# Performance work log

Hardware: AMD Instinct MI355X
Metric: run time of the kernel (lower is better)

Reference implementation:

```python
import jax, jax.numpy as jnp
import numpy as np


def setup_inputs() -> dict:
    key = jax.random.key(0)
    ks = jax.random.split(key, 32)
    def rn(i, shape, s=0.02):
        return jax.random.normal(ks[i], shape, dtype=jnp.float32) * s
    z = lambda n: jnp.zeros((n,), dtype=jnp.float32)
    return {
        'c2': rn(0, (8, 256, 112, 112), 1.0),
        'c3': rn(1, (8, 512, 56, 56), 1.0),
        'c4': rn(2, (8, 1024, 28, 28), 1.0),
        'c5': rn(3, (8, 2048, 14, 14), 1.0),
        'lat_w0': rn(4, (256, 256)),  'lat_b0': z(256),
        'lat_w1': rn(5, (512, 256)),  'lat_b1': z(256),
        'lat_w2': rn(6, (1024, 256)), 'lat_b2': z(256),
        'lat_w3': rn(7, (2048, 256)), 'lat_b3': z(256),
        'sp_w1': rn(8, (2048, 512)), 'sp_b1': z(512),
        'sp_w2': rn(9, (512, 4)),    'sp_b2': z(4),
        'qkv_w': rn(10, (256, 768)), 'qkv_b': z(768),
        'proj_w': rn(11, (256, 256)), 'proj_b': z(256),
        'gat_W': rn(12, (4, 256, 256)),
        'gat_a': rn(13, (4, 512)),
        'out_w': rn(14, (1024, 256)), 'out_b': z(256),
        'label_emb': rn(15, (80, 256), 1.0),
        'spec_w1': rn(16, (256, 128)), 'spec_b1': z(128),
        'spec_w2': rn(17, (128, 80)),  'spec_b2': z(80),
        'spat_w1': rn(18, (256, 128)), 'spat_b1': z(128),
        'spat_w2': rn(19, (128, 80)),  'spat_b2': z(80),
        'gate_w': rn(20, (256, 80)), 'gate_b': z(80),
        'unc_w': rn(21, (256, 80)),  'unc_b': z(80),
    }


def _forward(c2, c3, c4, c5,
             lat_w0, lat_b0, lat_w1, lat_b1, lat_w2, lat_b2, lat_w3, lat_b3,
             sp_w1, sp_b1, sp_w2, sp_b2,
             qkv_w, qkv_b, proj_w, proj_b,
             gat_W, gat_a, out_w, out_b, label_emb,
             spec_w1, spec_b1, spec_w2, spec_b2,
             spat_w1, spat_b1, spat_w2, spat_b2,
             gate_w, gate_b, unc_w, unc_b):
    B = c2.shape[0]
    L = label_emb.shape[0]
    C = 256
    # --- DynamicScaleAwareFPN ---
    pooled = c5.mean(axis=(2, 3))                                   # [B,2048]
    sw = jax.nn.softmax(jax.nn.relu(pooled @ sp_w1 + sp_b1) @ sp_w2 + sp_b2, axis=1)  # [B,4]
    H, W = c2.shape[2], c2.shape[3]
    feats = (c2, c3, c4, c5)
    lws = (lat_w0, lat_w1, lat_w2, lat_w3)
    lbs = (lat_b0, lat_b1, lat_b2, lat_b3)
    fused = jnp.zeros((B, C, H, W), dtype=c2.dtype)
    for i in range(4):  # fixed 4 scales
        l = jnp.einsum('bchw,cd->bdhw', feats[i], lws[i]) + lbs[i][None, :, None, None]
        if l.shape[2] != H or l.shape[3] != W:
            l = jax.image.resize(l, (B, C, H, W), method='bilinear')  # align_corners=False
        fused = fused + l * sw[:, i, None, None, None]
    # --- DeformableAttention (N=H*W > max_tokens=196 -> adaptive pool to 14x14) ---
    th = 14
    x = fused.reshape(B, C, th, H // th, th, W // th).mean(axis=(3, 5))  # exact adaptive avg pool
    x = x.reshape(B, C, th * th).transpose(0, 2, 1)                      # [B,196,C]
    N, nh, hd = th * th, 8, C // 8
    qkv = (x @ qkv_w + qkv_b).reshape(B, N, 3, nh, hd).transpose(2, 0, 3, 1, 4)
    q, k, v = qkv[0], qkv[1], qkv[2]                                     # [B,nh,N,hd]
    attn = jax.nn.softmax(jnp.einsum('bhnd,bhmd->bhnm', q, k) * (hd ** -0.5), axis=-1)
    xo = jnp.einsum('bhnm,bhmd->bhnd', attn, v).transpose(0, 2, 1, 3).reshape(B, N, C)
    xo = xo @ proj_w + proj_b
    gctx = xo.mean(axis=1)                                               # [B,C]
    # --- CrossLabelSemanticGraph (4 GAT heads) ---
    lf = label_emb[None] + gctx[:, None, :]                              # [B,L,C]
    def gat(Wm, avec):
        Wx = lf @ Wm                                                     # [B,L,C]
        # a([Wx_i ; Wx_j]) = Wx_i @ a1 + Wx_j @ a2  (avoids O(L^2*2C) tensor)
        s1 = Wx @ avec[:C]                                               # [B,L]
        s2 = Wx @ avec[C:]                                               # [B,L]
        e = jax.nn.leaky_relu(s1[:, :, None] + s2[:, None, :], 0.2)      # [B,L,L]
        att = jax.nn.softmax(e, axis=2)
        return att @ Wx, att
    heads, atts = jax.vmap(gat)(gat_W, gat_a)                            # [4,B,L,C],[4,B,L,L]
    concat = jnp.moveaxis(heads, 0, 2).reshape(B, L, 4 * C)              # head-order concat
    graph = concat @ out_w + out_b                                       # [B,L,C]
    agg = graph.mean(axis=1)                                             # [B,C]
    # --- SpectralSpatialFusion (dropout inactive at eval) ---
    spec = jax.nn.relu(agg @ spec_w1 + spec_b1) @ spec_w2 + spec_b2
    spat = jax.nn.relu(agg @ spat_w1 + spat_b1) @ spat_w2 + spat_b2
    gate = jax.nn.sigmoid(agg @ gate_w + gate_b)
    logits = gate * spec + (1.0 - gate) * spat
    # --- UncertaintyHead ---
    alpha = jax.nn.softplus(agg @ unc_w + unc_b) + 1.0
    unc = L / jnp.sum(alpha, axis=1, keepdims=True)
    return (logits, spec, spat, gate, unc, sw, atts)


def reference(c2, c3, c4, c5,
              lat_w0, lat_b0, lat_w1, lat_b1, lat_w2, lat_b2, lat_w3, lat_b3,
              sp_w1, sp_b1, sp_w2, sp_b2,
              qkv_w, qkv_b, proj_w, proj_b,
              gat_W, gat_a, out_w, out_b, label_emb,
              spec_w1, spec_b1, spec_w2, spec_b2,
              spat_w1, spat_b1, spat_w2, spat_b2,
              gate_w, gate_b, unc_w, unc_b):
    return _forward(c2, c3, c4, c5,
                    lat_w0, lat_b0, lat_w1, lat_b1, lat_w2, lat_b2, lat_w3, lat_b3,
                    sp_w1, sp_b1, sp_w2, sp_b2,
                    qkv_w, qkv_b, proj_w, proj_b,
                    gat_W, gat_a, out_w, out_b, label_emb,
                    spec_w1, spec_b1, spec_w2, spec_b2,
                    spat_w1, spat_b1, spat_w2, spat_b2,
                    gate_w, gate_b, unc_w, unc_b)
```

## Files before the change

kernel.cpp:

```cpp
#include <hip/hip_runtime.h>
#include <math.h>

typedef __attribute__((ext_vector_type(8))) short bshort8;
typedef __attribute__((ext_vector_type(4))) float f32x4;

#define DI __device__ __forceinline__

DI unsigned short f2bf(float x) {
    unsigned int u = __builtin_bit_cast(unsigned int, x);
    u += 0x7fffu + ((u >> 16) & 1u);
    return (unsigned short)(u >> 16);
}

DI bshort8 pack8(const float* v) {
    bshort8 r;
    #pragma unroll
    for (int j = 0; j < 8; j++) r[j] = (short)f2bf(v[j]);
    return r;
}

DI f32x4 mfma16(bshort8 a, bshort8 b, f32x4 c) {
    return __builtin_amdgcn_mfma_f32_16x16x32_bf16(a, b, c, 0, 0, 0);
}

__device__ const float W14[14][3] = {
    {0.875f, 0.125f, 0.f},
    {0.125f, 0.75f, 0.125f}, {0.125f, 0.75f, 0.125f}, {0.125f, 0.75f, 0.125f},
    {0.125f, 0.75f, 0.125f}, {0.125f, 0.75f, 0.125f}, {0.125f, 0.75f, 0.125f},
    {0.125f, 0.75f, 0.125f}, {0.125f, 0.75f, 0.125f}, {0.125f, 0.75f, 0.125f},
    {0.125f, 0.75f, 0.125f}, {0.125f, 0.75f, 0.125f}, {0.125f, 0.75f, 0.125f},
    {0.125f, 0.875f, 0.f}};
__device__ const float W28[14][4] = {
    {0.5f, 0.4375f, 0.0625f, 0.f},
    {0.0625f, 0.4375f, 0.4375f, 0.0625f}, {0.0625f, 0.4375f, 0.4375f, 0.0625f},
    {0.0625f, 0.4375f, 0.4375f, 0.0625f}, {0.0625f, 0.4375f, 0.4375f, 0.0625f},
    {0.0625f, 0.4375f, 0.4375f, 0.0625f}, {0.0625f, 0.4375f, 0.4375f, 0.0625f},
    {0.0625f, 0.4375f, 0.4375f, 0.0625f}, {0.0625f, 0.4375f, 0.4375f, 0.0625f},
    {0.0625f, 0.4375f, 0.4375f, 0.0625f}, {0.0625f, 0.4375f, 0.4375f, 0.0625f},
    {0.0625f, 0.4375f, 0.4375f, 0.0625f}, {0.0625f, 0.4375f, 0.4375f, 0.0625f},
    {0.0625f, 0.4375f, 0.5f, 0.f}};
__device__ const float W56[14][6] = {
    {0.25f, 0.25f, 0.25f, 0.21875f, 0.03125f, 0.f},
    {0.03125f, 0.21875f, 0.25f, 0.25f, 0.21875f, 0.03125f},
    {0.03125f, 0.21875f, 0.25f, 0.25f, 0.21875f, 0.03125f},
    {0.03125f, 0.21875f, 0.25f, 0.25f, 0.21875f, 0.03125f},
    {0.03125f, 0.21875f, 0.25f, 0.25f, 0.21875f, 0.03125f},
    {0.03125f, 0.21875f, 0.25f, 0.25f, 0.21875f, 0.03125f},
    {0.03125f, 0.21875f, 0.25f, 0.25f, 0.21875f, 0.03125f},
    {0.03125f, 0.21875f, 0.25f, 0.25f, 0.21875f, 0.03125f},
    {0.03125f, 0.21875f, 0.25f, 0.25f, 0.21875f, 0.03125f},
    {0.03125f, 0.21875f, 0.25f, 0.25f, 0.21875f, 0.03125f},
    {0.03125f, 0.21875f, 0.25f, 0.25f, 0.21875f, 0.03125f},
    {0.03125f, 0.21875f, 0.25f, 0.25f, 0.21875f, 0.03125f},
    {0.03125f, 0.21875f, 0.25f, 0.25f, 0.21875f, 0.03125f},
    {0.03125f, 0.21875f, 0.25f, 0.25f, 0.25f, 0.f}};

template <int N, int C, int TAPS>
DI void pool_body(const float* __restrict__ src, unsigned short* __restrict__ dst,
                  unsigned blk, unsigned t)
{
    unsigned id = blk * 256u + t;
    unsigned p = id / 196u;
    unsigned r = id - p * 196u;
    unsigned ti = r / 14u, tj = r - ti * 14u;
    unsigned b = p / C, cin = p - b * C;
    const float* plane = src + (size_t)p * (N * N);
    float acc = 0.f;
    if constexpr (N == 112) {
        const float4* p4 = (const float4*)(plane + (size_t)(ti * 8) * 112 + tj * 8);
        float4 rv[16];
        #pragma unroll
        for (int i = 0; i < 8; i++) { rv[2 * i] = p4[i * 28]; rv[2 * i + 1] = p4[i * 28 + 1]; }
        #pragma unroll
        for (int i = 0; i < 16; i++) acc += (rv[i].x + rv[i].y) + (rv[i].z + rv[i].w);
        acc *= (1.f / 64.f);
    } else {
        constexpr int STRIDE = N / 14;
        const float (*WT)[TAPS] = (N == 14) ? (const float (*)[TAPS])W14
                                : (N == 28) ? (const float (*)[TAPS])W28
                                            : (const float (*)[TAPS])W56;
        int hs = (int)(STRIDE * ti) - 1; if (hs < 0) hs = 0;
        int ws = (int)(STRIDE * tj) - 1; if (ws < 0) ws = 0;
        float wh[TAPS], ww[TAPS];
        #pragma unroll
        for (int i = 0; i < TAPS; i++) { wh[i] = WT[ti][i]; ww[i] = WT[tj][i]; }
        float rv[TAPS][TAPS];
        #pragma unroll
        for (int i = 0; i < TAPS; i++) {
            int hi = hs + i; if (hi > N - 1) hi = N - 1;
            const float* row = plane + (size_t)hi * N;
            #pragma unroll
            for (int j = 0; j < TAPS; j++) {
                int wj = ws + j; if (wj > N - 1) wj = N - 1;
                rv[i][j] = row[wj];
            }
        }
        #pragma unroll
        for (int i = 0; i < TAPS; i++) {
            float rs = 0.f;
            #pragma unroll
            for (int j = 0; j < TAPS; j++) rs += ww[j] * rv[i][j];
            acc += wh[i] * rs;
        }
    }
    dst[(size_t)cin * 1568 + b * 196 + r] = f2bf(acc);
}

DI void c5_mean_body(const float* __restrict__ c5, float* __restrict__ pooled,
                     unsigned blk, unsigned t)
{
    int wid = t >> 6, lane = t & 63;
    int p = blk * 4 + wid;
    const float* plane = c5 + (size_t)p * 196;
    float v = plane[lane] + plane[64 + lane] + plane[128 + lane];
    if (lane < 4) v += plane[192 + lane];
    #pragma unroll
    for (int off = 32; off > 0; off >>= 1) v += __shfl_xor(v, off, 64);
    if (lane == 0) pooled[p] = v * (1.f / 196.f);
}

__global__ __launch_bounds__(256) void pool_all(
    const float* __restrict__ c2, const float* __restrict__ c3,
    const float* __restrict__ c4, const float* __restrict__ c5,
    unsigned short* __restrict__ pf0, unsigned short* __restrict__ pf1,
    unsigned short* __restrict__ pf2, unsigned short* __restrict__ pf3,
    float* __restrict__ pooled)
{
    unsigned bx = blockIdx.x, t = threadIdx.x;
    if (bx < 1568u)       pool_body<112, 256, 8>(c2, pf0, bx, t);
    else if (bx < 4704u)  pool_body<56, 512, 6>(c3, pf1, bx - 1568u, t);
    else if (bx < 10976u) pool_body<28, 1024, 4>(c4, pf2, bx - 4704u, t);
    else if (bx < 23520u) pool_body<14, 2048, 3>(c5, pf3, bx - 10976u, t);
    else                  c5_mean_body(c5, pooled, bx - 23520u, t);
}

__global__ __launch_bounds__(512) void sw_part(
    const float* __restrict__ pooled, const float* __restrict__ sp_w1,
    float* __restrict__ partial,
    const float* __restrict__ gat_W, const float* __restrict__ gat_a,
    float* __restrict__ Wa)
{
    int t = threadIdx.x;
    if (blockIdx.y >= 8) {
        int e = (blockIdx.y - 8) * 8 + blockIdx.x;
        int h = e >> 2, q = e & 3;
        __shared__ float a1[256], a2[256];
        if (t < 256) { a1[t] = gat_a[h * 512 + t]; a2[t] = gat_a[h * 512 + 256 + t]; }
        __syncthreads();
        int w = t >> 6, lane = t & 63;
        #pragma unroll
        for (int ci = 0; ci < 8; ci++) {
            int c = q * 64 + w * 8 + ci;
            const float* row = gat_W + (size_t)h * 65536 + (size_t)c * 256;
            float p1 = 0.f, p2 = 0.f;
            #pragma unroll
            for (int jj = 0; jj < 4; jj++) {
                float v = row[lane + 64 * jj];
                p1 += v * a1[lane + 64 * jj];
                p2 += v * a2[lane + 64 * jj];
            }
            #pragma unroll
            for (int off = 32; off > 0; off >>= 1) {
                p1 += __shfl_xor(p1, off, 64);
                p2 += __shfl_xor(p2, off, 64);
            }
            if (lane == 0) { Wa[h * 512 + c] = p1; Wa[h * 512 + 256 + c] = p2; }
        }
        return;
    }
    int b = blockIdx.x, kc = blockIdx.y;
    __shared__ float ps[256];
    if (t < 256) ps[t] = pooled[b * 2048 + kc * 256 + t];
    __syncthreads();
    float acc = 0.f;
    const float* w = sp_w1 + (size_t)(kc * 256) * 512 + t;
    #pragma unroll 8
    for (int c = 0; c < 256; c++) acc += ps[c] * w[(size_t)c * 512];
    partial[((size_t)b * 8 + kc) * 512 + t] = acc;
}

__global__ __launch_bounds__(512) void sw_fin(
    const float* __restrict__ partial, const float* __restrict__ sp_b1,
    const float* __restrict__ sp_w2, const float* __restrict__ sp_b2,
    const float* __restrict__ lb0, const float* __restrict__ lb1,
    const float* __restrict__ lb2, const float* __restrict__ lb3,
    const float* __restrict__ lemb, const float* __restrict__ Wa,
    float* __restrict__ sw_out, float* __restrict__ xtok,
    float* __restrict__ ldot)
{
    int b = blockIdx.x, t = threadIdx.x;
    __shared__ float h[512];
    __shared__ float s4s[4];
    __shared__ float swl[4];
    __shared__ float bf_s[256];
    float a = sp_b1[t];
    #pragma unroll
    for (int kc = 0; kc < 8; kc++) a += partial[((size_t)b * 8 + kc) * 512 + t];
    h[t] = fmaxf(a, 0.f);
    __syncthreads();
    int wv = t >> 6, lane = t & 63;
    if (wv < 4) {
        float acc = 0.f;
        #pragma unroll
        for (int i = 0; i < 8; i++) {
            int idx = lane + 64 * i;
            acc += h[idx] * sp_w2[idx * 4 + wv];
        }
        #pragma unroll
        for (int off = 32; off > 0; off >>= 1) acc += __shfl_xor(acc, off, 64);
        if (lane == 0) s4s[wv] = acc + sp_b2[wv];
    }
    __syncthreads();
    if (t == 0) {
        float mx = fmaxf(fmaxf(s4s[0], s4s[1]), fmaxf(s4s[2], s4s[3]));
        float e0 = expf(s4s[0] - mx), e1 = expf(s4s[1] - mx);
        float e2 = expf(s4s[2] - mx), e3 = expf(s4s[3] - mx);
        float inv = 1.f / (e0 + e1 + e2 + e3);
        swl[0] = e0 * inv; swl[1] = e1 * inv; swl[2] = e2 * inv; swl[3] = e3 * inv;
        for (int o = 0; o < 4; o++) sw_out[b * 4 + o] = swl[o];
    }
    __syncthreads();
    if (t < 256)
        bf_s[t] = swl[0] * lb0[t] + swl[1] * lb1[t] + swl[2] * lb2[t] + swl[3] * lb3[t];
    {
        int pair = t >> 6;
        #pragma unroll
        for (int r = 0; r < 10; r++) {
            int l = b * 10 + r;
            const float* le = lemb + l * 256 + lane * 4;
            const float* wa = Wa + pair * 256 + lane * 4;
            float p = le[0] * wa[0] + le[1] * wa[1] + le[2] * wa[2] + le[3] * wa[3];
            #pragma unroll
            for (int off = 32; off > 0; off >>= 1) p += __shfl_xor(p, off, 64);
            if (lane == 0) ldot[l * 8 + pair] = p;
        }
    }
    __syncthreads();
    int c = t & 255, half = t >> 8;
    float bv = bf_s[c];
    float* xb = xtok + (size_t)b * 196 * 256 + c;
    for (int r = half; r < 196; r += 2) xb[(size_t)r * 256] = bv;
}

__global__ __launch_bounds__(256) void lateral_slice(
    const unsigned short* __restrict__ pf0, const unsigned short* __restrict__ pf1,
    const unsigned short* __restrict__ pf2, const unsigned short* __restrict__ pf3,
    const float* __restrict__ w0, const float* __restrict__ w1,
    const float* __restrict__ w2, const float* __restrict__ w3,
    const float* __restrict__ sw, float* __restrict__ xtok)
{
    const int sArr[8]    = {0, 1, 2, 2, 3, 3, 3, 3};
    const int koffArr[8] = {0, 0, 0, 512, 0, 512, 1024, 1536};
    const int klenArr[8] = {256, 512, 512, 512, 512, 512, 512, 512};
    int sl = blockIdx.y;
    int s = sArr[sl], koff = koffArr[sl], klen = klenArr[sl];
    const unsigned short* pf = (s == 0) ? pf0 : (s == 1) ? pf1 : (s == 2) ? pf2 : pf3;
    const float* W  = (s == 0) ? w0  : (s == 1) ? w1  : (s == 2) ? w2  : w3;

    int mt = blockIdx.x % 49, nt = blockIdx.x / 49;
    int m0 = mt * 32, n0 = nt * 64;
    __shared__ alignas(16) unsigned short As[1024];
    __shared__ alignas(16) unsigned short Bs[2048];
    int t = threadIdx.x, lane = t & 63, wid = t >> 6;
    int wm = wid >> 1, wn = wid & 1;
    f32x4 acc0 = {0, 0, 0, 0}, acc1 = {0, 0, 0, 0};

    int f = t & 63;
    int mA = m0 + ((t >> 6) & 1) * 16 + (f & 15);
    int kbA = (f >> 4) * 8;
    int nB = n0 + (t >> 6) * 16 + (f & 15);
    int kbB = (f >> 4) * 8;

    unsigned short ark[8];
    float br[8];
    auto loadA = [&](int k0) {
        if (t < 128) {
            const unsigned short* base = pf + (size_t)(koff + k0 + kbA) * 1568 + mA;
            #pragma unroll
            for (int j = 0; j < 8; j++) ark[j] = base[(size_t)j * 1568];
        }
    };
    auto loadB = [&](int k0) {
        const float* base = W + (size_t)(koff + k0 + kbB) * 256 + nB;
        #pragma unroll
        for (int j = 0; j < 8; j++) br[j] = base[(size_t)j * 256];
    };

    loadA(0); loadB(0);
    for (int k0 = 0; k0 < klen; k0 += 32) {
        if (t < 128) {
            bshort8 v8;
            #pragma unroll
            for (int j = 0; j < 8; j++) v8[j] = (short)ark[j];
            *(bshort8*)&As[(((t >> 6) & 1) * 512 + f * 8)] = v8;
        }
        *(bshort8*)&Bs[((t >> 6) * 512 + f * 8)] = pack8(br);
        __syncthreads();
        if (k0 + 32 < klen) { loadA(k0 + 32); loadB(k0 + 32); }
        bshort8 av = *(const bshort8*)&As[wm * 512 + lane * 8];
        bshort8 bv0 = *(const bshort8*)&Bs[(wn * 2 + 0) * 512 + lane * 8];
        bshort8 bv1 = *(const bshort8*)&Bs[(wn * 2 + 1) * 512 + lane * 8];
        acc0 = mfma16(av, bv0, acc0);
        acc1 = mfma16(av, bv1, acc1);
        __syncthreads();
    }
    int col0 = n0 + wn * 32 + (lane & 15);
    int rbase = m0 + wm * 16 + ((lane >> 4) << 2);
    #pragma unroll
    for (int r = 0; r < 4; r++) {
        int m = rbase + r;
        float swv = sw[(m / 196) * 4 + s];
        atomicAdd(&xtok[(size_t)m * 256 + col0], acc0[r] * swv);
        atomicAdd(&xtok[(size_t)m * 256 + col0 + 16], acc1[r] * swv);
    }
}

template <bool B_IS_KXN>
__global__ __launch_bounds__(256) void gemm_kernel(
    const float* __restrict__ Ab, int lda, long long sAy, long long sAz,
    const float* __restrict__ Bb, int ldb, long long sBy, long long sBz,
    float* __restrict__ Cb, int ldc, long long sCy, long long sCz,
    const float* __restrict__ bias, int M, int N, int K,
    float alpha, int mtiles)
{
    const float* A = Ab + blockIdx.y * sAy + blockIdx.z * sAz;
    const float* B = Bb + blockIdx.y * sBy + blockIdx.z * sBz;
    float* C = Cb + blockIdx.y * sCy + blockIdx.z * sCz;
    int mt = blockIdx.x % mtiles, nt = blockIdx.x / mtiles;
    int m0 = mt * 32, n0 = nt * 64;
    __shared__ alignas(16) unsigned short As[1024];
    __shared__ alignas(16) unsigned short Bs[2048];
    int t = threadIdx.x, lane = t & 63, wid = t >> 6;
    int wm = wid >> 1, wn = wid & 1;
    f32x4 acc0 = {0, 0, 0, 0}, acc1 = {0, 0, 0, 0};

    int f = t & 63;
    int mA = m0 + ((t >> 6) & 1) * 16 + (f & 15);
    int kbA = (f >> 4) * 8;
    int nB = n0 + (t >> 6) * 16 + (f & 15);
    int kbB = (f >> 4) * 8;

    float ar[8], br[8];
    auto loadA = [&](int k0) {
        if (t < 128) {
            int kb = k0 + kbA;
            if (mA < M && kb + 8 <= K) {
                const float4* p = (const float4*)(A + (size_t)mA * lda + kb);
                float4 u = p[0], v = p[1];
                ar[0] = u.x; ar[1] = u.y; ar[2] = u.z; ar[3] = u.w;
                ar[4] = v.x; ar[5] = v.y; ar[6] = v.z; ar[7] = v.w;
            } else {
                #pragma unroll
                for (int j = 0; j < 8; j++) {
                    int k = kb + j;
                    ar[j] = (mA < M && k < K) ? A[(size_t)mA * lda + k] : 0.f;
                }
            }
        }
    };
    auto loadB = [&](int k0) {
        int kb = k0 + kbB;
        if constexpr (B_IS_KXN) {
            #pragma unroll
            for (int j = 0; j < 8; j++) {
                int k = kb + j;
                br[j] = (k < K && nB < N) ? B[(size_t)k * ldb + nB] : 0.f;
            }
        } else {
            if (nB < N && kb + 8 <= K) {
                const float4* p = (const float4*)(B + (size_t)nB * ldb + kb);
                float4 u = p[0], v = p[1];
                br[0] = u.x; br[1] = u.y; br[2] = u.z; br[3] = u.w;
                br[4] = v.x; br[5] = v.y; br[6] = v.z; br[7] = v.w;
            } else {
                #pragma unroll
                for (int j = 0; j < 8; j++) {
                    int k = kb + j;
                    br[j] = (nB < N && k < K) ? B[(size_t)nB * ldb + k] : 0.f;
                }
            }
        }
    };

    loadA(0); loadB(0);
    for (int k0 = 0; k0 < K; k0 += 32) {
        if (t < 128) *(bshort8*)&As[(((t >> 6) & 1) * 512 + f * 8)] = pack8(ar);
        *(bshort8*)&Bs[((t >> 6) * 512 + f * 8)] = pack8(br);
        __syncthreads();
        if (k0 + 32 < K) { loadA(k0 + 32); loadB(k0 + 32); }
        bshort8 av = *(const bshort8*)&As[wm * 512 + lane * 8];
        bshort8 bv0 = *(const bshort8*)&Bs[(wn * 2 + 0) * 512 + lane * 8];
        bshort8 bv1 = *(const bshort8*)&Bs[(wn * 2 + 1) * 512 + lane * 8];
        acc0 = mfma16(av, bv0, acc0);
        acc1 = mfma16(av, bv1, acc1);
        __syncthreads();
    }
    int col0 = n0 + wn * 32 + (lane & 15);
    int rbase = m0 + wm * 16 + ((lane >> 4) << 2);
    #pragma unroll
    for (int r = 0; r < 4; r++) {
        int m = rbase + r;
        if (m < M) {
            if (col0 < N) {
                float v = acc0[r] * alpha;
                if (bias) v += bias[col0];
                C[(size_t)m * ldc + col0] = v;
            }
            int c1 = col0 + 16;
            if (c1 < N) {
                float v = acc1[r] * alpha;
                if (bias) v += bias[c1];
                C[(size_t)m * ldc + c1] = v;
            }
        }
    }
}

__global__ __launch_bounds__(256) void fused_attn(
    const float* __restrict__ qkv, float* __restrict__ xo)
{
    int mt = blockIdx.x, h = blockIdx.y, b = blockIdx.z;
    const float* Qb = qkv + (size_t)b * 150528 + h * 32;
    const float* Kb = Qb + 256;
    const float* Vb = Qb + 512;

    __shared__ alignas(16) unsigned short As[1024];
    __shared__ alignas(16) unsigned short Bs[2048];
    __shared__ float Ss[32 * 256];

    int t = threadIdx.x, lane = t & 63, wid = t >> 6;
    int wm = wid >> 1, wn = wid & 1;
    int f = t & 63;
    int m0 = mt * 32;

    if (t < 128) {
        float ar[8];
        int mA = m0 + ((t >> 6) & 1) * 16 + (f & 15);
        int kb = (f >> 4) * 8;
        if (mA < 196) {
            const float4* p = (const float4*)(Qb + (size_t)mA * 768 + kb);
            float4 u = p[0], v = p[1];
            ar[0] = u.x; ar[1] = u.y; ar[2] = u.z; ar[3] = u.w;
            ar[4] = v.x; ar[5] = v.y; ar[6] = v.z; ar[7] = v.w;
        } else {
            #pragma unroll
            for (int j = 0; j < 8; j++) ar[j] = 0.f;
        }
        *(bshort8*)&As[(((t >> 6) & 1) * 512 + f * 8)] = pack8(ar);
    }

    {
        int nBl = (t >> 6) * 16 + (f & 15);
        int kbB = (f >> 4) * 8;
        float br[8];
        auto loadB = [&](int g) {
            int key = g * 64 + nBl;
            if (key < 196) {
                const float4* p = (const float4*)(Kb + (size_t)key * 768 + kbB);
                float4 u = p[0], v = p[1];
                br[0] = u.x; br[1] = u.y; br[2] = u.z; br[3] = u.w;
                br[4] = v.x; br[5] = v.y; br[6] = v.z; br[7] = v.w;
            } else {
                #pragma unroll
                for (int j = 0; j < 8; j++) br[j] = 0.f;
            }
        };
        loadB(0);
        for (int g = 0; g < 4; g++) {
            __syncthreads();
            *(bshort8*)&Bs[((t >> 6) * 512 + f * 8)] = pack8(br);
            __syncthreads();
            if (g < 3) loadB(g + 1);
            f32x4 acc0 = {0, 0, 0, 0}, acc1 = {0, 0, 0, 0};
            bshort8 av = *(const bshort8*)&As[wm * 512 + lane * 8];
            bshort8 bv0 = *(const bshort8*)&Bs[(wn * 2 + 0) * 512 + lane * 8];
            bshort8 bv1 = *(const bshort8*)&Bs[(wn * 2 + 1) * 512 + lane * 8];
            acc0 = mfma16(av, bv0, acc0);
            acc1 = mfma16(av, bv1, acc1);
            int col0 = g * 64 + wn * 32 + (lane & 15);
            int rbase = wm * 16 + ((lane >> 4) << 2);
            #pragma unroll
            for (int r = 0; r < 4; r++) {
                Ss[(rbase + r) * 256 + col0]      = acc0[r] * 0.17677669529663687f;
                Ss[(rbase + r) * 256 + col0 + 16] = acc1[r] * 0.17677669529663687f;
            }
        }
    }
    __syncthreads();

    {
        #pragma unroll
        for (int i = 0; i < 8; i++) {
            float* p = Ss + (wid * 8 + i) * 256;
            float v0 = p[lane], v1 = p[64 + lane], v2 = p[128 + lane];
            float v3 = (lane < 4) ? p[192 + lane] : -1e30f;
            float mx = fmaxf(fmaxf(v0, v1), fmaxf(v2, v3));
            #pragma unroll
            for (int off = 32; off > 0; off >>= 1) mx = fmaxf(mx, __shfl_xor(mx, off, 64));
            float e0 = expf(v0 - mx), e1 = expf(v1 - mx), e2 = expf(v2 - mx);
            float e3 = (lane < 4) ? expf(v3 - mx) : 0.f;
            float sum = e0 + e1 + e2 + e3;
            #pragma unroll
            for (int off = 32; off > 0; off >>= 1) sum += __shfl_xor(sum, off, 64);
            float inv = 1.f / sum;
            p[lane] = e0 * inv;
            p[64 + lane] = e1 * inv;
            p[128 + lane] = e2 * inv;
            if (lane < 4) p[192 + lane] = e3 * inv;
            else          p[192 + lane] = 0.f;
        }
    }
    __syncthreads();

    {
        f32x4 acc0 = {0, 0, 0, 0}, acc1 = {0, 0, 0, 0};
        int nBl = (t >> 6) * 16 + (f & 15);
        int kbB = (f >> 4) * 8;
        int mAl = ((t >> 6) & 1) * 16 + (f & 15);
        int kbA = (f >> 4) * 8;
        float ar[8], br[8];
        auto loadA = [&](int k0) {
            if (t < 128) {
                #pragma unroll
                for (int j = 0; j < 8; j++) ar[j] = Ss[mAl * 256 + k0 + kbA + j];
            }
        };
        auto loadB = [&](int k0) {
            #pragma unroll
            for (int j = 0; j < 8; j++) {
                int k = k0 + kbB + j;
                br[j] = (k < 196 && nBl < 32) ? Vb[(size_t)k * 768 + nBl] : 0.f;
            }
        };
        loadA(0); loadB(0);
        for (int k0 = 0; k0 < 256; k0 += 32) {
            __syncthreads();
            if (t < 128) *(bshort8*)&As[(((t >> 6) & 1) * 512 + f * 8)] = pack8(ar);
            *(bshort8*)&Bs[((t >> 6) * 512 + f * 8)] = pack8(br);
            __syncthreads();
            if (k0 + 32 < 256) { loadA(k0 + 32); loadB(k0 + 32); }
            bshort8 av = *(const bshort8*)&As[wm * 512 + lane * 8];
            bshort8 bv0 = *(const bshort8*)&Bs[(wn * 2 + 0) * 512 + lane * 8];
            bshort8 bv1 = *(const bshort8*)&Bs[(wn * 2 + 1) * 512 + lane * 8];
            acc0 = mfma16(av, bv0, acc0);
            acc1 = mfma16(av, bv1, acc1);
        }
        int col0 = wn * 32 + (lane & 15);
        int rbase = wm * 16 + ((lane >> 4) << 2);
        if (col0 < 32) {
            #pragma unroll
            for (int r = 0; r < 4; r++) {
                int m = m0 + rbase + r;
                if (m < 196) {
                    xo[((size_t)b * 196 + m) * 256 + h * 32 + col0]      = acc0[r];
                    xo[((size_t)b * 196 + m) * 256 + h * 32 + col0 + 16] = acc1[r];
                }
            }
        }
    }
}

__global__ __launch_bounds__(1024) void tail1(
    const float* __restrict__ xo, const float* __restrict__ proj_w,
    const float* __restrict__ proj_b,
    const float* __restrict__ gat_W, const float* __restrict__ lemb,
    const float* __restrict__ Wa, const float* __restrict__ ldot,
    float* __restrict__ atts, float* __restrict__ hm_g)
{
    int b = blockIdx.x >> 2, h = blockIdx.x & 3;
    int t = threadIdx.x, lane = t & 63, wv = t >> 6;
    __shared__ float red[1024];
    __shared__ float xm[256];
    __shared__ float gctx_s[256];
    __shared__ float gdot_s[2];
    __shared__ float s12h[160];
    __shared__ float am_s[80];
    __shared__ float av_s[256];

    {
        int c = t & 255, sl = t >> 8;
        const float* base = xo + ((size_t)b * 196 + sl * 49) * 256 + c;
        float s = 0.f;
        #pragma unroll 7
        for (int i = 0; i < 49; i++) s += base[(size_t)i * 256];
        red[t] = s;
    }
    if (t < 80) am_s[t] = 0.f;
    __syncthreads();
    if (t < 256) xm[t] = (red[t] + red[256 + t] + red[512 + t] + red[768 + t]) * (1.f / 196.f);
    __syncthreads();

    {
        int n = t & 255, ks = t >> 8;
        float acc = 0.f;
        const float* w = proj_w + (size_t)(ks * 64) * 256 + n;
        #pragma unroll 8
        for (int i = 0; i < 64; i++) acc += xm[ks * 64 + i] * w[(size_t)i * 256];
        red[t] = acc;
    }
    __syncthreads();
    if (t < 256) gctx_s[t] = proj_b[t] + red[t] + red[256 + t] + red[512 + t] + red[768 + t];
    __syncthreads();

    if (wv < 2) {
        int pair = h * 2 + wv;
        const float* wa = Wa + pair * 256 + lane * 4;
        float p = gctx_s[lane * 4] * wa[0] + gctx_s[lane * 4 + 1] * wa[1]
                + gctx_s[lane * 4 + 2] * wa[2] + gctx_s[lane * 4 + 3] * wa[3];
        #pragma unroll
        for (int off = 32; off > 0; off >>= 1) p += __shfl_xor(p, off, 64);
        if (lane == 0) gdot_s[wv] = p;
    }
    __syncthreads();
    if (t < 160) {
        int q = t / 80, l = t - q * 80;
        s12h[t] = ldot[l * 8 + h * 2 + q] + gdot_s[q];
    }
    __syncthreads();

    {
        #pragma unroll
        for (int rr = 0; rr < 5; rr++) {
            int i = rr * 16 + wv;
            float s1i = s12h[i];
            const float* s2 = s12h + 80;
            float v0 = s1i + s2[lane]; v0 = v0 > 0.f ? v0 : 0.2f * v0;
            float v1 = -1e30f;
            if (lane < 16) { v1 = s1i + s2[64 + lane]; v1 = v1 > 0.f ? v1 : 0.2f * v1; }
            float mx = fmaxf(v0, v1);
            #pragma unroll
            for (int off = 32; off > 0; off >>= 1) mx = fmaxf(mx, __shfl_xor(mx, off, 64));
            float e0 = expf(v0 - mx), e1 = (lane < 16) ? expf(v1 - mx) : 0.f;
            float sum = e0 + e1;
            #pragma unroll
            for (int off = 32; off > 0; off >>= 1) sum += __shfl_xor(sum, off, 64);
            float inv = 1.f / sum;
            float* orow = atts + (size_t)h * 51200 + b * 6400 + i * 80;
            float p0 = e0 * inv;
            orow[lane] = p0;
            atomicAdd(&am_s[lane], p0);
            if (lane < 16) {
                float p1 = e1 * inv;
                orow[64 + lane] = p1;
                atomicAdd(&am_s[64 + lane], p1);
            }
        }
    }
    __syncthreads();

    {
        int n = t & 255, ks = t >> 8;
        float acc = 0.f;
        const float* le = lemb + n;
        #pragma unroll 5
        for (int l = ks * 20; l < ks * 20 + 20; l++) acc += am_s[l] * le[(size_t)l * 256];
        red[t] = acc;
    }
    __syncthreads();
    if (t < 256)
        av_s[t] = (red[t] + red[256 + t] + red[512 + t] + red[768 + t]) * (1.f / 80.f)
                + gctx_s[t];
    __syncthreads();
    {
        int n = t & 255, ks = t >> 8;
        float acc = 0.f;
        const float* w = gat_W + (size_t)h * 65536 + (size_t)(ks * 64) * 256 + n;
        #pragma unroll 8
        for (int i = 0; i < 64; i++) acc += av_s[ks * 64 + i] * w[(size_t)i * 256];
        red[t] = acc;
    }
    __syncthreads();
    if (t < 256)
        hm_g[(b * 4 + h) * 256 + t] = red[t] + red[256 + t] + red[512 + t] + red[768 + t];
}

__global__ __launch_bounds__(1024) void tail2(
    const float* __restrict__ hm_g,
    const float* __restrict__ out_w, const float* __restrict__ out_b,
    const float* __restrict__ spec_w1, const float* __restrict__ spec_b1,
    const float* __restrict__ spec_w2, const float* __restrict__ spec_b2,
    const float* __restrict__ spat_w1, const float* __restrict__ spat_b1,
    const float* __restrict__ spat_w2, const float* __restrict__ spat_b2,
    const float* __restrict__ gate_w, const float* __restrict__ gate_b,
    const float* __restrict__ unc_w, const float* __restrict__ unc_b,
    float* __restrict__ out)
{
    int b = blockIdx.x, t = threadIdx.x;
    __shared__ float red[1024];
    __shared__ float as_s[256];
    __shared__ float hb_s[256];
    __shared__ float fv_s[320];

    {
        int n = t & 255, ks = t >> 8;
        float acc = 0.f;
        const float* hv = hm_g + b * 1024 + ks * 256;
        const float* w = out_w + (size_t)(ks * 256) * 256 + n;
        #pragma unroll 8
        for (int k = 0; k < 256; k++) acc += hv[k] * w[(size_t)k * 256];
        red[t] = acc;
    }
    __syncthreads();
    if (t < 256) as_s[t] = out_b[t] + red[t] + red[256 + t] + red[512 + t] + red[768 + t];
    __syncthreads();

    {
        int u = t & 255, ks = t >> 8;
        int which = u >> 7, oo = u & 127;
        const float* w1 = which ? spat_w1 : spec_w1;
        float acc = 0.f;
        #pragma unroll 8
        for (int i = 0; i < 64; i++) {
            int k = ks * 64 + i;
            acc += as_s[k] * w1[(size_t)k * 128 + oo];
        }
        red[t] = acc;
    }
    __syncthreads();
    if (t < 256) {
        int which = t >> 7, oo = t & 127;
        const float* b1 = which ? spat_b1 : spec_b1;
        hb_s[t] = fmaxf(red[t] + red[256 + t] + red[512 + t] + red[768 + t] + b1[oo], 0.f);
    }
    __syncthreads();

    if (t < 960) {
        int sub = t / 320, u = t - sub * 320;
        int head = u / 80, o = u - head * 80;
        const float* wp; const float* src; int K;
        if (head == 0)      { wp = spec_w2; src = hb_s;       K = 128; }
        else if (head == 1) { wp = spat_w2; src = hb_s + 128; K = 128; }
        else if (head == 2) { wp = gate_w;  src = as_s;       K = 256; }
        else                { wp = unc_w;   src = as_s;       K = 256; }
        int k0 = (K * sub) / 3, k1 = (K * (sub + 1)) / 3;
        float acc = 0.f;
        for (int k = k0; k < k1; k++) acc += src[k] * wp[(size_t)k * 80 + o];
        red[sub * 320 + u] = acc;
    }
    __syncthreads();
    if (t < 320) {
        int head = t / 80, o = t - head * 80;
        const float* bp = head == 0 ? spec_b2 : head == 1 ? spat_b2 : head == 2 ? gate_b : unc_b;
        fv_s[t] = red[t] + red[320 + t] + red[640 + t] + bp[o];
    }
    __syncthreads();

    if (t < 80) {
        float sp = fv_s[t], st2 = fv_s[80 + t], gz = fv_s[160 + t], uz = fv_s[240 + t];
        float g = 1.f / (1.f + expf(-gz));
        out[b * 80 + t] = g * sp + (1.f - g) * st2;
        out[640 + b * 80 + t] = sp;
        out[1280 + b * 80 + t] = st2;
        out[1920 + b * 80 + t] = g;
        red[t] = log1pf(expf(uz)) + 1.f;
    }
    __syncthreads();
    if (t == 0) {
        float s = 0.f;
        for (int l = 0; l < 80; l++) s += red[l];
        out[2560 + b] = 80.f / s;
    }
}

extern "C" void kernel_launch(void* const* d_in, const int* in_sizes, int n_in,
                              void* d_out, int out_size, void* d_ws, size_t ws_size,
                              hipStream_t stream)
{
    (void)in_sizes; (void)n_in; (void)out_size; (void)ws_size;
    const float* c2 = (const float*)d_in[0];
    const float* c3 = (const float*)d_in[1];
    const float* c4 = (const float*)d_in[2];
    const float* c5 = (const float*)d_in[3];
    const float* lat_w0 = (const float*)d_in[4];
    const float* lat_b0 = (const float*)d_in[5];
    const float* lat_w1 = (const float*)d_in[6];
    const float* lat_b1 = (const float*)d_in[7];
    const float* lat_w2 = (const float*)d_in[8];
    const float* lat_b2 = (const float*)d_in[9];
    const float* lat_w3 = (const float*)d_in[10];
    const float* lat_b3 = (const float*)d_in[11];
    const float* sp_w1 = (const float*)d_in[12];
    const float* sp_b1 = (const float*)d_in[13];
    const float* sp_w2 = (const float*)d_in[14];
    const float* sp_b2 = (const float*)d_in[15];
    const float* qkv_w = (const float*)d_in[16];
    const float* qkv_b = (const float*)d_in[17];
    const float* proj_w = (const float*)d_in[18];
    const float* proj_b = (const float*)d_in[19];
    const float* gat_W = (const float*)d_in[20];
    const float* gat_a = (const float*)d_in[21];
    const float* out_w = (const float*)d_in[22];
    const float* out_b = (const float*)d_in[23];
    const float* label_emb = (const float*)d_in[24];
    const float* spec_w1 = (const float*)d_in[25];
    const float* spec_b1 = (const float*)d_in[26];
    const float* spec_w2 = (const float*)d_in[27];
    const float* spec_b2 = (const float*)d_in[28];
    const float* spat_w1 = (const float*)d_in[29];
    const float* spat_b1 = (const float*)d_in[30];
    const float* spat_w2 = (const float*)d_in[31];
    const float* spat_b2 = (const float*)d_in[32];
    const float* gate_w = (const float*)d_in[33];
    const float* gate_b = (const float*)d_in[34];
    const float* unc_w = (const float*)d_in[35];
    const float* unc_b = (const float*)d_in[36];

    float* out = (float*)d_out;
    float* ws = (float*)d_ws;

    unsigned short* pf0 = (unsigned short*)(ws + 0);
    unsigned short* pf1 = (unsigned short*)(ws + 401408);
    unsigned short* pf2 = (unsigned short*)(ws + 1204224);
    unsigned short* pf3 = (unsigned short*)(ws + 2809856);
    float* pooled = ws + 6021120;
    float* swpart = ws + 6039552;
    float* Wa     = ws + 6072320;
    float* ldot   = ws + 6074368;
    float* qkv    = ws + 0;
    float* xo     = ws + 3662848;
    float* hm_g   = ws + 4253696;
    float* xtok   = ws + 6106112;

    float* swp  = out + 2568;
    float* atts = out + 2600;

    pool_all<<<27616, 256, 0, stream>>>(c2, c3, c4, c5, pf0, pf1, pf2, pf3, pooled);
    sw_part<<<dim3(8, 10), 512, 0, stream>>>(pooled, sp_w1, swpart, gat_W, gat_a, Wa);
    sw_fin<<<8, 512, 0, stream>>>(swpart, sp_b1, sp_w2, sp_b2,
                                  lat_b0, lat_b1, lat_b2, lat_b3,
                                  label_emb, Wa, swp, xtok, ldot);
    lateral_slice<<<dim3(196, 8), 256, 0, stream>>>(pf0, pf1, pf2, pf3,
                                                    lat_w0, lat_w1, lat_w2, lat_w3,
                                                    swp, xtok);
    gemm_kernel<true><<<dim3(49 * 12, 1, 1), 256, 0, stream>>>(
        xtok, 256, 0, 0, qkv_w, 768, 0, 0, qkv, 768, 0, 0,
        qkv_b, 1568, 768, 256, 1.f, 49);
    fused_attn<<<dim3(7, 8, 8), 256, 0, stream>>>(qkv, xo);
    tail1<<<32, 1024, 0, stream>>>(xo, proj_w, proj_b, gat_W, label_emb,
                                   Wa, ldot, atts, hm_g);
    tail2<<<8, 1024, 0, stream>>>(hm_g, out_w, out_b,
                                  spec_w1, spec_b1, spec_w2, spec_b2,
                                  spat_w1, spat_b1, spat_w2, spat_b2,
                                  gate_w, gate_b, unc_w, unc_b, out);
}
```

Baseline: 494.1 us.

## Stage pooling planes in LDS and fuse c5 mean with c5 pooling

The c3/c4/c5 adaptive-pooling branches now load whole input planes into shared memory with coalesced float4 loads and compute the overlapping weighted taps from LDS, one block per plane. Before, each thread gathered its taps straight from global memory. The c5 branch also reuses its loaded plane for the global mean, so c5 is no longer read twice. The cost is more idle threads (196 of 256 active), a 12.5KB LDS allocation on every block including the c2 path, and extra syncthreads.

```diff
diff --git a/kernel.cpp b/kernel.cpp
--- a/kernel.cpp
+++ b/kernel.cpp
@@ -55,68 +55,23 @@
     {0.03125f, 0.21875f, 0.25f, 0.25f, 0.21875f, 0.03125f},
     {0.03125f, 0.21875f, 0.25f, 0.25f, 0.25f, 0.f}};
 
-template <int N, int C, int TAPS>
-DI void pool_body(const float* __restrict__ src, unsigned short* __restrict__ dst,
-                  unsigned blk, unsigned t)
+DI void pool_body112(const float* __restrict__ src, unsigned short* __restrict__ dst,
+                     unsigned blk, unsigned t)
 {
     unsigned id = blk * 256u + t;
     unsigned p = id / 196u;
     unsigned r = id - p * 196u;
     unsigned ti = r / 14u, tj = r - ti * 14u;
-    unsigned b = p / C, cin = p - b * C;
-    const float* plane = src + (size_t)p * (N * N);
+    unsigned b = p >> 8, cin = p & 255u;
+    const float* plane = src + (size_t)p * 12544;
+    const float4* p4 = (const float4*)(plane + (size_t)(ti * 8) * 112 + tj * 8);
+    float4 rv[16];
+    #pragma unroll
+    for (int i = 0; i < 8; i++) { rv[2 * i] = p4[i * 28]; rv[2 * i + 1] = p4[i * 28 + 1]; }
     float acc = 0.f;
-    if constexpr (N == 112) {
-        const float4* p4 = (const float4*)(plane + (size_t)(ti * 8) * 112 + tj * 8);
-        float4 rv[16];
-        #pragma unroll
-        for (int i = 0; i < 8; i++) { rv[2 * i] = p4[i * 28]; rv[2 * i + 1] = p4[i * 28 + 1]; }
-        #pragma unroll
-        for (int i = 0; i < 16; i++) acc += (rv[i].x + rv[i].y) + (rv[i].z + rv[i].w);
-        acc *= (1.f / 64.f);
-    } else {
-        constexpr int STRIDE = N / 14;
-        const float (*WT)[TAPS] = (N == 14) ? (const float (*)[TAPS])W14
-                                : (N == 28) ? (const float (*)[TAPS])W28
-                                            : (const float (*)[TAPS])W56;
-        int hs = (int)(STRIDE * ti) - 1; if (hs < 0) hs = 0;
-        int ws = (int)(STRIDE * tj) - 1; if (ws < 0) ws = 0;
-        float wh[TAPS], ww[TAPS];
-        #pragma unroll
-        for (int i = 0; i < TAPS; i++) { wh[i] = WT[ti][i]; ww[i] = WT[tj][i]; }
-        float rv[TAPS][TAPS];
-        #pragma unroll
-        for (int i = 0; i < TAPS; i++) {
-            int hi = hs + i; if (hi > N - 1) hi = N - 1;
-            const float* row = plane + (size_t)hi * N;
-            #pragma unroll
-            for (int j = 0; j < TAPS; j++) {
-                int wj = ws + j; if (wj > N - 1) wj = N - 1;
-                rv[i][j] = row[wj];
-            }
-        }
-        #pragma unroll
-        for (int i = 0; i < TAPS; i++) {
-            float rs = 0.f;
-            #pragma unroll
-            for (int j = 0; j < TAPS; j++) rs += ww[j] * rv[i][j];
-            acc += wh[i] * rs;
-        }
-    }
-    dst[(size_t)cin * 1568 + b * 196 + r] = f2bf(acc);
-}
-
-DI void c5_mean_body(const float* __restrict__ c5, float* __restrict__ pooled,
-                     unsigned blk, unsigned t)
-{
-    int wid = t >> 6, lane = t & 63;
-    int p = blk * 4 + wid;
-    const float* plane = c5 + (size_t)p * 196;
-    float v = plane[lane] + plane[64 + lane] + plane[128 + lane];
-    if (lane < 4) v += plane[192 + lane];
     #pragma unroll
-    for (int off = 32; off > 0; off >>= 1) v += __shfl_xor(v, off, 64);
-    if (lane == 0) pooled[p] = v * (1.f / 196.f);
+    for (int i = 0; i < 16; i++) acc += (rv[i].x + rv[i].y) + (rv[i].z + rv[i].w);
+    dst[(size_t)cin * 1568 + b * 196 + r] = f2bf(acc * (1.f / 64.f));
 }
 
 __global__ __launch_bounds__(256) void pool_all(
@@ -126,12 +81,114 @@
     unsigned short* __restrict__ pf2, unsigned short* __restrict__ pf3,
     float* __restrict__ pooled)
 {
+    __shared__ alignas(16) float ls[3136];
     unsigned bx = blockIdx.x, t = threadIdx.x;
-    if (bx < 1568u)       pool_body<112, 256, 8>(c2, pf0, bx, t);
-    else if (bx < 4704u)  pool_body<56, 512, 6>(c3, pf1, bx - 1568u, t);
-    else if (bx < 10976u) pool_body<28, 1024, 4>(c4, pf2, bx - 4704u, t);
-    else if (bx < 23520u) pool_body<14, 2048, 3>(c5, pf3, bx - 10976u, t);
-    else                  c5_mean_body(c5, pooled, bx - 23520u, t);
+
+    if (bx < 1568u) {
+        pool_body112(c2, pf0, bx, t);
+        return;
+    }
+    if (bx < 5664u) {
+        unsigned p = bx - 1568u;
+        unsigned b = p >> 9, cin = p & 511u;
+        const float* plane = c3 + (size_t)p * 3136;
+        float4* l4 = (float4*)ls;
+        const float4* s4 = (const float4*)plane;
+        for (int i = t; i < 784; i += 256) l4[i] = s4[i];
+        __syncthreads();
+        if (t < 196) {
+            int ti = t / 14, tj = t - ti * 14;
+            int hs = 4 * ti - 1; if (hs < 0) hs = 0;
+            int ws = 4 * tj - 1; if (ws < 0) ws = 0;
+            float acc = 0.f;
+            #pragma unroll
+            for (int i = 0; i < 6; i++) {
+                int hi = hs + i; if (hi > 55) hi = 55;
+                const float* row = ls + hi * 56;
+                float rs = 0.f;
+                #pragma unroll
+                for (int j = 0; j < 6; j++) {
+                    int wj = ws + j; if (wj > 55) wj = 55;
+                    rs += W56[tj][j] * row[wj];
+                }
+                acc += W56[ti][i] * rs;
+            }
+            pf1[(size_t)cin * 1568 + b * 196 + t] = f2bf(acc);
+        }
+        return;
+    }
+    if (bx < 13856u) {
+        unsigned p = bx - 5664u;
+        unsigned b = p >> 10, cin = p & 1023u;
+        const float* plane = c4 + (size_t)p * 784;
+        float4* l4 = (float4*)ls;
+        const float4* s4 = (const float4*)plane;
+        if (t < 196) l4[t] = s4[t];
+        __syncthreads();
+        if (t < 196) {
+            int ti = t / 14, tj = t - ti * 14;
+            int hs = 2 * ti - 1; if (hs < 0) hs = 0;
+            int ws = 2 * tj - 1; if (ws < 0) ws = 0;
+            float acc = 0.f;
+            #pragma unroll
+            for (int i = 0; i < 4; i++) {
+                int hi = hs + i; if (hi > 27) hi = 27;
+                const float* row = ls + hi * 28;
+                float rs = 0.f;
+                #pragma unroll
+                for (int j = 0; j < 4; j++) {
+                    int wj = ws + j; if (wj > 27) wj = 27;
+                    rs += W28[tj][j] * row[wj];
+                }
+                acc += W28[ti][i] * rs;
+            }
+            pf2[(size_t)cin * 1568 + b * 196 + t] = f2bf(acc);
+        }
+        return;
+    }
+    {
+        unsigned g = bx - 13856u;
+        int wid = t >> 6, lane = t & 63;
+        unsigned p = g * 4 + wid;
+        unsigned b = p >> 11, cin = p & 2047u;
+        const float* plane = c5 + (size_t)p * 196;
+        float a0 = plane[lane];
+        float a1 = plane[64 + lane];
+        float a2 = plane[128 + lane];
+        float a3 = (lane < 4) ? plane[192 + lane] : 0.f;
+        float* lw = ls + wid * 200;
+        lw[lane] = a0; lw[64 + lane] = a1; lw[128 + lane] = a2;
+        if (lane < 4) lw[192 + lane] = a3;
+        float v = a0 + a1 + a2 + a3;
+        #pragma unroll
+        for (int off = 32; off > 0; off >>= 1) v += __shfl_xor(v, off, 64);
+        if (lane == 0) pooled[p] = v * (1.f / 196.f);
+        __syncthreads();
+        unsigned short* dst = pf3 + (size_t)cin * 1568 + b * 196;
+        #pragma unroll
+        for (int rr = 0; rr < 4; rr++) {
+            int r = rr * 64 + lane;
+            if (r < 196) {
+                int ti = r / 14, tj = r - ti * 14;
+                int hs = ti - 1; if (hs < 0) hs = 0;
+                int ws = tj - 1; if (ws < 0) ws = 0;
+                float acc = 0.f;
+                #pragma unroll
+                for (int i = 0; i < 3; i++) {
+                    int hi = hs + i; if (hi > 13) hi = 13;
+                    const float* row = lw + hi * 14;
+                    float rs = 0.f;
+                    #pragma unroll
+                    for (int j = 0; j < 3; j++) {
+                        int wj = ws + j; if (wj > 13) wj = 13;
+                        rs += W14[tj][j] * row[wj];
+                    }
+                    acc += W14[ti][i] * rs;
+                }
+                dst[r] = f2bf(acc);
+            }
+        }
+    }
 }
 
 __global__ __launch_bounds__(512) void sw_part(
@@ -824,7 +881,7 @@
     float* swp  = out + 2568;
     float* atts = out + 2600;
 
-    pool_all<<<27616, 256, 0, stream>>>(c2, c3, c4, c5, pf0, pf1, pf2, pf3, pooled);
+    pool_all<<<17952, 256, 0, stream>>>(c2, c3, c4, c5, pf0, pf1, pf2, pf3, pooled);
     sw_part<<<dim3(8, 10), 512, 0, stream>>>(pooled, sp_w1, swpart, gat_W, gat_a, Wa);
     sw_fin<<<8, 512, 0, stream>>>(swpart, sp_b1, sp_w2, sp_b2,
                                   lat_b0, lat_b1, lat_b2, lat_b3,
```

Result: faster. 460.7 us (-6.8%).
